# Kernel optimization log

Measured on AMD Instinct MI355X. Metric: run time of the kernel, lower is better.

Reference implementation:

```python
import jax, jax.numpy as jnp
import numpy as np


def gcn_conv(x, W, b, src, dst, n_nodes):
    """PyG-style GCNConv: x' = D^{-1/2}(A+I)D^{-1/2} X W + b, with self-loops added."""
    h = x @ W  # [N, F_out]
    # add self-loops
    loop = jnp.arange(n_nodes, dtype=src.dtype)
    s = jnp.concatenate([src, loop])  # [E+N]
    d = jnp.concatenate([dst, loop])  # [E+N]
    # symmetric normalization: deg counted over incoming edges (incl. self-loops)
    deg = jax.ops.segment_sum(jnp.ones_like(d, dtype=h.dtype), d, num_segments=n_nodes)
    dinv = jnp.where(deg > 0, jax.lax.rsqrt(deg), 0.0)
    coef = dinv[s] * dinv[d]  # [E+N]
    msg = h[s] * coef[:, None]  # gather + scale, [E+N, F_out]
    out = jax.ops.segment_sum(msg, d, num_segments=n_nodes)  # scatter-add
    return out + b


def setup_inputs() -> dict:
    key = jax.random.key(0)
    ks = jax.random.split(key, 6)
    N, E, F_IN, F_HID, F_OUT = 50000, 800000, 128, 128, 64
    x = jax.random.normal(ks[0], (N, F_IN), dtype=jnp.float32)
    edge_index = jax.random.randint(ks[1], (2, E), 0, N, dtype=jnp.int64)
    W0 = jax.random.normal(ks[2], (F_IN, F_HID), dtype=jnp.float32) * (F_IN ** -0.5)
    b0 = jnp.zeros((F_HID,), dtype=jnp.float32)
    W1 = jax.random.normal(ks[3], (F_HID, F_HID), dtype=jnp.float32) * (F_HID ** -0.5)
    b1 = jnp.zeros((F_HID,), dtype=jnp.float32)
    W2 = jax.random.normal(ks[4], (F_HID, F_OUT), dtype=jnp.float32) * (F_HID ** -0.5)
    b2 = jnp.zeros((F_OUT,), dtype=jnp.float32)
    return {"x": x, "edge_index": edge_index, "W0": W0, "b0": b0,
            "W1": W1, "b1": b1, "W2": W2, "b2": b2}


def reference(x, edge_index, W0, b0, W1, b1, W2, b2):
    n_nodes = x.shape[0]
    src, dst = edge_index[0], edge_index[1]
    # hidden GCNConv layers with relu (dropout is identity in eval mode)
    h = jax.nn.relu(gcn_conv(x, W0, b0, src, dst, n_nodes))
    h = jax.nn.relu(gcn_conv(h, W1, b1, src, dst, n_nodes))
    # final conv, no activation
    return gcn_conv(h, W2, b2, src, dst, n_nodes)
```

## Files before the change

kernel.cpp:

```cpp
#include <hip/hip_runtime.h>
#include <hip/hip_fp16.h>
#include <type_traits>

#define F_IN 128
#define NPART 8

typedef _Float16 f16x8 __attribute__((ext_vector_type(8)));
typedef _Float16 f16x4 __attribute__((ext_vector_type(4)));
typedef _Float16 f16x2 __attribute__((ext_vector_type(2)));
typedef float f32x4 __attribute__((ext_vector_type(4)));


__global__ void setup_kernel(const float* __restrict__ W0, const float* __restrict__ W1,
                             const float* __restrict__ W2, __half* __restrict__ Wt0,
                             __half* __restrict__ Wt1, __half* __restrict__ Wt2,
                             int* __restrict__ deg, int N) {
    int idx = blockIdx.x * 256 + threadIdx.x;
    if (idx < 16384) {
        int k = idx >> 7, n = idx & 127;
        Wt0[n * 128 + k] = __float2half_rn(W0[idx]);
    } else if (idx < 32768) {
        int j = idx - 16384;
        int k = j >> 7, n = j & 127;
        Wt1[n * 128 + k] = __float2half_rn(W1[j]);
    } else if (idx < 40960) {
        int j = idx - 32768;
        int k = j >> 6, n = j & 63;
        Wt2[n * 128 + k] = __float2half_rn(W2[j]);
    }
    if (idx < N) deg[idx] = 0;
}


__global__ __launch_bounds__(256) void deg_part_kernel(
    const int* __restrict__ dst, int* __restrict__ deg, int E, int psize)
{
    const int part  = blockIdx.x % NPART;
    const int bslot = blockIdx.x / NPART;
    const int nb    = gridDim.x / NPART;
    const int lo = part * psize;
    const int hi = lo + psize;
    for (int e = bslot * 256 + threadIdx.x; e < E; e += nb * 256) {
        int d = dst[e];
        if (d >= lo && d < hi) atomicAdd(&deg[d], 1);
    }
}


__global__ void scan_blocks(const int* __restrict__ deg, int* __restrict__ rp,
                            int* __restrict__ bsum, int N) {
    __shared__ int tmp[256];
    int t = threadIdx.x, i = blockIdx.x * 256 + t;
    int v = (i < N) ? deg[i] : 0;
    tmp[t] = v;
    __syncthreads();
    for (int off = 1; off < 256; off <<= 1) {
        int a = (t >= off) ? tmp[t - off] : 0;
        __syncthreads();
        tmp[t] += a;
        __syncthreads();
    }
    if (i < N) rp[i] = tmp[t] - v;
    if (t == 255) bsum[blockIdx.x] = tmp[255];
}

__global__ void scan_bsum(int* __restrict__ bsum, int nb) {
    __shared__ int tmp[256];
    int t = threadIdx.x;
    int v = (t < nb) ? bsum[t] : 0;
    tmp[t] = v;
    __syncthreads();
    for (int off = 1; off < 256; off <<= 1) {
        int a = (t >= off) ? tmp[t - off] : 0;
        __syncthreads();
        tmp[t] += a;
        __syncthreads();
    }
    if (t < nb) bsum[t] = tmp[t] - v;
}

__global__ void add_offsets_kernel(int* __restrict__ rp, const int* __restrict__ bsum,
                                   int* __restrict__ cursor, const int* __restrict__ deg,
                                   float* __restrict__ dinv, int N) {
    int i = blockIdx.x * 256 + threadIdx.x;
    if (i < N) {
        int r = rp[i] + bsum[blockIdx.x];
        rp[i] = r;
        cursor[i] = r;
        dinv[i] = rsqrtf((float)(deg[i] + 1));
    }
}

__global__ __launch_bounds__(256) void build_csr_kernel(
    const int* __restrict__ src, const int* __restrict__ dst,
    int* __restrict__ cursor, unsigned short* __restrict__ csr_src,
    int E, int psize)
{
    const int part  = blockIdx.x % NPART;
    const int bslot = blockIdx.x / NPART;
    const int nb    = gridDim.x / NPART;
    const int lo = part * psize;
    const int hi = lo + psize;
    for (int e = bslot * 256 + threadIdx.x; e < E; e += nb * 256) {
        int d = dst[e];
        if (d >= lo && d < hi) {
            int pos = atomicAdd(&cursor[d], 1);
            csr_src[pos] = (unsigned short)src[e];
        }
    }
}


template<int BN, typename XT>
__global__ __launch_bounds__(256) void gemm_mfma_kernel(
    const XT* __restrict__ X, const __half* __restrict__ Wt,
    const float* __restrict__ dinv, __half* __restrict__ g, int N)
{
    constexpr int K  = 128;
    constexpr int KP = K + 8;
    constexpr int NT = BN / 16;
    __shared__ __half Ws[BN * KP];

    const int tid = threadIdx.x;
    for (int c = tid; c < BN * (K / 8); c += 256) {
        int n  = c >> 4;
        int k8 = c & 15;
        *(f16x8*)&Ws[n * KP + k8 * 8] =
            *(const f16x8*)((const _Float16*)Wt + n * K + k8 * 8);
    }
    __syncthreads();

    const int lane = tid & 63;
    const int w    = tid >> 6;
    const int lrow = lane & 15;
    const int kg   = lane >> 4;
    const int row0 = blockIdx.x * 64 + w * 16;
    const int gr   = row0 + lrow;

    f32x4 acc[NT];
    #pragma unroll
    for (int t = 0; t < NT; ++t) acc[t] = (f32x4){0.f, 0.f, 0.f, 0.f};

    #pragma unroll
    for (int ks = 0; ks < 4; ++ks) {
        const int k0 = ks * 32 + kg * 8;
        f16x8 a = {};
        if constexpr (sizeof(XT) == 4) {
            if (gr < N) {
                const float* p = (const float*)X + (size_t)gr * K + k0;
                float4 x0 = *(const float4*)p;
                float4 x1 = *(const float4*)(p + 4);
                a[0] = (_Float16)x0.x; a[1] = (_Float16)x0.y;
                a[2] = (_Float16)x0.z; a[3] = (_Float16)x0.w;
                a[4] = (_Float16)x1.x; a[5] = (_Float16)x1.y;
                a[6] = (_Float16)x1.z; a[7] = (_Float16)x1.w;
            }
        } else {
            if (gr < N)
                a = *(const f16x8*)((const _Float16*)X + (size_t)gr * K + k0);
        }
        #pragma unroll
        for (int t = 0; t < NT; ++t) {
            f16x8 b = *(const f16x8*)&Ws[(t * 16 + lrow) * KP + k0];
            acc[t] = __builtin_amdgcn_mfma_f32_16x16x32_f16(a, b, acc[t], 0, 0, 0);
        }
    }

    #pragma unroll
    for (int r = 0; r < 4; ++r) {
        int m = row0 + kg * 4 + r;
        if (m < N) {
            float dn = dinv[m];
            #pragma unroll
            for (int t = 0; t < NT; ++t)
                g[(size_t)m * BN + t * 16 + lrow] = __float2half_rn(dn * acc[t][r]);
        }
    }
}


template<int FO, bool RELU, typename OT>
__global__ __launch_bounds__(256) void aggregate_kernel(
    const __half* __restrict__ g, const int* __restrict__ rp, const int* __restrict__ deg,
    const unsigned short* __restrict__ csr, const float* __restrict__ dinv,
    const float* __restrict__ bias, OT* __restrict__ out, int N)
{
    constexpr int PER = FO / 32;
    using VT = typename std::conditional<PER == 4, f16x4, f16x2>::type;

    int gid  = blockIdx.x * 256 + threadIdx.x;
    int node = gid >> 5;
    int lane = gid & 31;
    if (node >= N) return;

    int start = rp[node];
    int dg    = deg[node];

    const _Float16* gb = (const _Float16*)g + (size_t)lane * PER;

    float a[PER];
    {
        VT v = *(const VT*)(gb + (size_t)node * FO);
        #pragma unroll
        for (int p = 0; p < PER; ++p) a[p] = (float)v[p];
    }

    int j = 0;
    for (; j + 3 < dg; j += 4) {
        int s0 = csr[start + j];
        int s1 = csr[start + j + 1];
        int s2 = csr[start + j + 2];
        int s3 = csr[start + j + 3];
        VT v0 = *(const VT*)(gb + (size_t)s0 * FO);
        VT v1 = *(const VT*)(gb + (size_t)s1 * FO);
        VT v2 = *(const VT*)(gb + (size_t)s2 * FO);
        VT v3 = *(const VT*)(gb + (size_t)s3 * FO);
        #pragma unroll
        for (int p = 0; p < PER; ++p)
            a[p] += ((float)v0[p] + (float)v1[p]) + ((float)v2[p] + (float)v3[p]);
    }
    for (; j < dg; ++j) {
        int s0 = csr[start + j];
        VT v0 = *(const VT*)(gb + (size_t)s0 * FO);
        #pragma unroll
        for (int p = 0; p < PER; ++p) a[p] += (float)v0[p];
    }

    float dn = dinv[node];
    float o[PER];
    #pragma unroll
    for (int p = 0; p < PER; ++p) {
        o[p] = fmaf(dn, a[p], bias[lane * PER + p]);
        if (RELU) o[p] = fmaxf(o[p], 0.f);
    }

    if constexpr (sizeof(OT) == 2) {
        VT h;
        #pragma unroll
        for (int p = 0; p < PER; ++p) h[p] = (_Float16)o[p];
        *(VT*)((_Float16*)out + (size_t)node * FO + lane * PER) = h;
    } else {
        float* op = (float*)out + (size_t)node * FO + lane * PER;
        if constexpr (PER == 4) {
            *(float4*)op = make_float4(o[0], o[1], o[2], o[3]);
        } else {
            *(float2*)op = make_float2(o[0], o[1]);
        }
    }
}


extern "C" void kernel_launch(void* const* d_in, const int* in_sizes, int n_in,
                              void* d_out, int out_size, void* d_ws, size_t ws_size,
                              hipStream_t stream) {
    const float* x  = (const float*)d_in[0];
    const int*   ei = (const int*)d_in[1];
    const float* W0 = (const float*)d_in[2];
    const float* b0 = (const float*)d_in[3];
    const float* W1 = (const float*)d_in[4];
    const float* b1 = (const float*)d_in[5];
    const float* W2 = (const float*)d_in[6];
    const float* b2 = (const float*)d_in[7];
    float* out = (float*)d_out;

    const int N = in_sizes[0] / F_IN;
    const int E = in_sizes[1] / 2;
    const int* src = ei;
    const int* dst = ei + E;

    char* ws = (char*)d_ws;
    size_t off = 0;
    __half* bufA  = (__half*)(ws + off); off += (size_t)N * 128 * 2;
    __half* bufB  = (__half*)(ws + off); off += (size_t)N * 128 * 2;
    float* dinv   = (float*)(ws + off); off += (size_t)N * 4;
    int*   deg    = (int*)  (ws + off); off += (size_t)N * 4;
    int*   rowptr = (int*)  (ws + off); off += (size_t)N * 4;
    int*   cursor = (int*)  (ws + off); off += (size_t)N * 4;
    int*   bsum   = (int*)  (ws + off); off += 256 * 4;
    unsigned short* csr = (unsigned short*)(ws + off); off += (size_t)E * 2;
    off = (off + 255) & ~(size_t)255;
    __half* wt0 = (__half*)(ws + off); off += 128 * 128 * 2;
    __half* wt1 = (__half*)(ws + off); off += 128 * 128 * 2;
    __half* wt2 = (__half*)(ws + off); off += 64 * 128 * 2;

    const int nb_nodes = (N + 255) / 256;
    const int nb_setup = (((N > 40960 ? N : 40960) + 255) / 256);
    const int nb_aggr  = (N * 32 + 255) / 256;
    const int nb_gemm  = (N + 63) / 64;
    const int psize    = (N + NPART - 1) / NPART;

    setup_kernel<<<nb_setup, 256, 0, stream>>>(W0, W1, W2, wt0, wt1, wt2, deg, N);
    deg_part_kernel<<<NPART * 128, 256, 0, stream>>>(dst, deg, E, psize);
    scan_blocks<<<nb_nodes, 256, 0, stream>>>(deg, rowptr, bsum, N);
    scan_bsum<<<1, 256, 0, stream>>>(bsum, nb_nodes);
    add_offsets_kernel<<<nb_nodes, 256, 0, stream>>>(rowptr, bsum, cursor, deg, dinv, N);
    build_csr_kernel<<<NPART * 128, 256, 0, stream>>>(src, dst, cursor, csr, E, psize);

    gemm_mfma_kernel<128, float><<<nb_gemm, 256, 0, stream>>>(x, wt0, dinv, bufA, N);
    aggregate_kernel<128, true, __half><<<nb_aggr, 256, 0, stream>>>(bufA, rowptr, deg, csr, dinv, b0, bufB, N);

    gemm_mfma_kernel<128, __half><<<nb_gemm, 256, 0, stream>>>(bufB, wt1, dinv, bufA, N);
    aggregate_kernel<128, true, __half><<<nb_aggr, 256, 0, stream>>>(bufA, rowptr, deg, csr, dinv, b1, bufB, N);

    gemm_mfma_kernel<64, __half><<<nb_gemm, 256, 0, stream>>>(bufB, wt2, dinv, bufA, N);
    aggregate_kernel<64, false, float><<<nb_aggr, 256, 0, stream>>>(bufA, rowptr, deg, csr, dinv, b2, out, N);
}
```

Measured before the change: 211.1 us.

## Fuse aggregation with next-layer GEMM via shared memory and merge scan kernels

Each hidden-layer aggregation now writes its ReLU'd fp16 rows into an LDS tile, and the next layer's MFMA GEMM runs in the same block. This removes the intermediate global write and re-read of the activations and two kernel launches. The scan_bsum kernel is dropped: each add_offsets block reduces the preceding block sums itself. In exchange, aggregation gets 64 nodes per block with 8 nodes per pass instead of a flat grid. The extra LDS may also cut occupancy.

```diff
diff --git a/kernel.cpp b/kernel.cpp
--- a/kernel.cpp
+++ b/kernel.cpp
@@ -64,27 +64,21 @@
     if (t == 255) bsum[blockIdx.x] = tmp[255];
 }
 
-__global__ void scan_bsum(int* __restrict__ bsum, int nb) {
+__global__ void add_offsets_kernel(int* __restrict__ rp, const int* __restrict__ bsum,
+                                   int* __restrict__ cursor, const int* __restrict__ deg,
+                                   float* __restrict__ dinv, int N, int nb) {
     __shared__ int tmp[256];
     int t = threadIdx.x;
-    int v = (t < nb) ? bsum[t] : 0;
-    tmp[t] = v;
+    tmp[t] = (t < nb && t < (int)blockIdx.x) ? bsum[t] : 0;
     __syncthreads();
-    for (int off = 1; off < 256; off <<= 1) {
-        int a = (t >= off) ? tmp[t - off] : 0;
+    for (int s = 128; s > 0; s >>= 1) {
+        if (t < s) tmp[t] += tmp[t + s];
         __syncthreads();
-        tmp[t] += a;
-        __syncthreads();
-    }
-    if (t < nb) bsum[t] = tmp[t] - v;
-}
-
-__global__ void add_offsets_kernel(int* __restrict__ rp, const int* __restrict__ bsum,
-                                   int* __restrict__ cursor, const int* __restrict__ deg,
-                                   float* __restrict__ dinv, int N) {
-    int i = blockIdx.x * 256 + threadIdx.x;
+    }
+    int base = tmp[0];
+    int i = blockIdx.x * 256 + t;
     if (i < N) {
-        int r = rp[i] + bsum[blockIdx.x];
+        int r = rp[i] + base;
         rp[i] = r;
         cursor[i] = r;
         dinv[i] = rsqrtf((float)(deg[i] + 1));
@@ -111,13 +105,13 @@
 }
 
 
-template<int BN, typename XT>
-__global__ __launch_bounds__(256) void gemm_mfma_kernel(
-    const XT* __restrict__ X, const __half* __restrict__ Wt,
+__global__ __launch_bounds__(256) void gemm_mfma_l0_kernel(
+    const float* __restrict__ X, const __half* __restrict__ Wt,
     const float* __restrict__ dinv, __half* __restrict__ g, int N)
 {
     constexpr int K  = 128;
     constexpr int KP = K + 8;
+    constexpr int BN = 128;
     constexpr int NT = BN / 16;
     __shared__ __half Ws[BN * KP];
 
@@ -145,19 +139,14 @@
     for (int ks = 0; ks < 4; ++ks) {
         const int k0 = ks * 32 + kg * 8;
         f16x8 a = {};
-        if constexpr (sizeof(XT) == 4) {
-            if (gr < N) {
-                const float* p = (const float*)X + (size_t)gr * K + k0;
-                float4 x0 = *(const float4*)p;
-                float4 x1 = *(const float4*)(p + 4);
-                a[0] = (_Float16)x0.x; a[1] = (_Float16)x0.y;
-                a[2] = (_Float16)x0.z; a[3] = (_Float16)x0.w;
-                a[4] = (_Float16)x1.x; a[5] = (_Float16)x1.y;
-                a[6] = (_Float16)x1.z; a[7] = (_Float16)x1.w;
-            }
-        } else {
-            if (gr < N)
-                a = *(const f16x8*)((const _Float16*)X + (size_t)gr * K + k0);
+        if (gr < N) {
+            const float* p = X + (size_t)gr * K + k0;
+            float4 x0 = *(const float4*)p;
+            float4 x1 = *(const float4*)(p + 4);
+            a[0] = (_Float16)x0.x; a[1] = (_Float16)x0.y;
+            a[2] = (_Float16)x0.z; a[3] = (_Float16)x0.w;
+            a[4] = (_Float16)x1.x; a[5] = (_Float16)x1.y;
+            a[6] = (_Float16)x1.z; a[7] = (_Float16)x1.w;
         }
         #pragma unroll
         for (int t = 0; t < NT; ++t) {
@@ -179,15 +168,116 @@
 }
 
 
-template<int FO, bool RELU, typename OT>
-__global__ __launch_bounds__(256) void aggregate_kernel(
+template<int BN>
+__global__ __launch_bounds__(256) void fused_agg_gemm_kernel(
+    const __half* __restrict__ gin, const int* __restrict__ rp,
+    const int* __restrict__ deg, const unsigned short* __restrict__ csr,
+    const float* __restrict__ dinv, const float* __restrict__ bias,
+    const __half* __restrict__ Wt, __half* __restrict__ gout, int N)
+{
+    constexpr int K  = 128;
+    constexpr int KP = K + 8;
+    constexpr int XP = K + 8;
+    constexpr int NT = BN / 16;
+    __shared__ __half Ws[BN * KP];
+    __shared__ __half Xl[64 * XP];
+
+    const int tid = threadIdx.x;
+    for (int c = tid; c < BN * (K / 8); c += 256) {
+        int n  = c >> 4;
+        int k8 = c & 15;
+        *(f16x8*)&Ws[n * KP + k8 * 8] =
+            *(const f16x8*)((const _Float16*)Wt + n * K + k8 * 8);
+    }
+
+    const int row0 = blockIdx.x * 64;
+    const int grp  = tid >> 5;
+    const int ln   = tid & 31;
+    const _Float16* gb = (const _Float16*)gin + (size_t)ln * 4;
+
+    #pragma unroll 2
+    for (int pass = 0; pass < 8; ++pass) {
+        int nloc = pass * 8 + grp;
+        int node = row0 + nloc;
+        float o[4] = {0.f, 0.f, 0.f, 0.f};
+        if (node < N) {
+            int start = rp[node];
+            int dg    = deg[node];
+            f16x4 sv = *(const f16x4*)(gb + (size_t)node * 128);
+            float a[4];
+            #pragma unroll
+            for (int p = 0; p < 4; ++p) a[p] = (float)sv[p];
+            int j = 0;
+            for (; j + 3 < dg; j += 4) {
+                int s0 = csr[start + j];
+                int s1 = csr[start + j + 1];
+                int s2 = csr[start + j + 2];
+                int s3 = csr[start + j + 3];
+                f16x4 v0 = *(const f16x4*)(gb + (size_t)s0 * 128);
+                f16x4 v1 = *(const f16x4*)(gb + (size_t)s1 * 128);
+                f16x4 v2 = *(const f16x4*)(gb + (size_t)s2 * 128);
+                f16x4 v3 = *(const f16x4*)(gb + (size_t)s3 * 128);
+                #pragma unroll
+                for (int p = 0; p < 4; ++p)
+                    a[p] += ((float)v0[p] + (float)v1[p]) + ((float)v2[p] + (float)v3[p]);
+            }
+            for (; j < dg; ++j) {
+                int s0 = csr[start + j];
+                f16x4 v0 = *(const f16x4*)(gb + (size_t)s0 * 128);
+                #pragma unroll
+                for (int p = 0; p < 4; ++p) a[p] += (float)v0[p];
+            }
+            float dn = dinv[node];
+            #pragma unroll
+            for (int p = 0; p < 4; ++p)
+                o[p] = fmaxf(fmaf(dn, a[p], bias[ln * 4 + p]), 0.f);
+        }
+        f16x4 h;
+        #pragma unroll
+        for (int p = 0; p < 4; ++p) h[p] = (_Float16)o[p];
+        *(f16x4*)&Xl[nloc * XP + ln * 4] = h;
+    }
+    __syncthreads();
+
+    const int lane = tid & 63;
+    const int w    = tid >> 6;
+    const int lrow = lane & 15;
+    const int kg   = lane >> 4;
+
+    f32x4 acc[NT];
+    #pragma unroll
+    for (int t = 0; t < NT; ++t) acc[t] = (f32x4){0.f, 0.f, 0.f, 0.f};
+
+    #pragma unroll
+    for (int ks = 0; ks < 4; ++ks) {
+        const int k0 = ks * 32 + kg * 8;
+        f16x8 a = *(const f16x8*)&Xl[(w * 16 + lrow) * XP + k0];
+        #pragma unroll
+        for (int t = 0; t < NT; ++t) {
+            f16x8 b = *(const f16x8*)&Ws[(t * 16 + lrow) * KP + k0];
+            acc[t] = __builtin_amdgcn_mfma_f32_16x16x32_f16(a, b, acc[t], 0, 0, 0);
+        }
+    }
+
+    #pragma unroll
+    for (int r = 0; r < 4; ++r) {
+        int m = row0 + w * 16 + kg * 4 + r;
+        if (m < N) {
+            float dn = dinv[m];
+            #pragma unroll
+            for (int t = 0; t < NT; ++t)
+                gout[(size_t)m * BN + t * 16 + lrow] = __float2half_rn(dn * acc[t][r]);
+        }
+    }
+}
+
+
+__global__ __launch_bounds__(256) void aggregate_final_kernel(
     const __half* __restrict__ g, const int* __restrict__ rp, const int* __restrict__ deg,
     const unsigned short* __restrict__ csr, const float* __restrict__ dinv,
-    const float* __restrict__ bias, OT* __restrict__ out, int N)
-{
-    constexpr int PER = FO / 32;
-    using VT = typename std::conditional<PER == 4, f16x4, f16x2>::type;
-
+    const float* __restrict__ bias, float* __restrict__ out, int N)
+{
+    constexpr int FO = 64, PER = 2;
     int gid  = blockIdx.x * 256 + threadIdx.x;
     int node = gid >> 5;
     int lane = gid & 31;
@@ -200,7 +290,7 @@
 
     float a[PER];
     {
-        VT v = *(const VT*)(gb + (size_t)node * FO);
+        f16x2 v = *(const f16x2*)(gb + (size_t)node * FO);
         #pragma unroll
         for (int p = 0; p < PER; ++p) a[p] = (float)v[p];
     }
@@ -211,42 +301,26 @@
         int s1 = csr[start + j + 1];
         int s2 = csr[start + j + 2];
         int s3 = csr[start + j + 3];
-        VT v0 = *(const VT*)(gb + (size_t)s0 * FO);
-        VT v1 = *(const VT*)(gb + (size_t)s1 * FO);
-        VT v2 = *(const VT*)(gb + (size_t)s2 * FO);
-        VT v3 = *(const VT*)(gb + (size_t)s3 * FO);
+        f16x2 v0 = *(const f16x2*)(gb + (size_t)s0 * FO);
+        f16x2 v1 = *(const f16x2*)(gb + (size_t)s1 * FO);
+        f16x2 v2 = *(const f16x2*)(gb + (size_t)s2 * FO);
+        f16x2 v3 = *(const f16x2*)(gb + (size_t)s3 * FO);
         #pragma unroll
         for (int p = 0; p < PER; ++p)
             a[p] += ((float)v0[p] + (float)v1[p]) + ((float)v2[p] + (float)v3[p]);
     }
     for (; j < dg; ++j) {
         int s0 = csr[start + j];
-        VT v0 = *(const VT*)(gb + (size_t)s0 * FO);
+        f16x2 v0 = *(const f16x2*)(gb + (size_t)s0 * FO);
         #pragma unroll
         for (int p = 0; p < PER; ++p) a[p] += (float)v0[p];
     }
 
     float dn = dinv[node];
-    float o[PER];
-    #pragma unroll
-    for (int p = 0; p < PER; ++p) {
-        o[p] = fmaf(dn, a[p], bias[lane * PER + p]);
-        if (RELU) o[p] = fmaxf(o[p], 0.f);
-    }
-
-    if constexpr (sizeof(OT) == 2) {
-        VT h;
-        #pragma unroll
-        for (int p = 0; p < PER; ++p) h[p] = (_Float16)o[p];
-        *(VT*)((_Float16*)out + (size_t)node * FO + lane * PER) = h;
-    } else {
-        float* op = (float*)out + (size_t)node * FO + lane * PER;
-        if constexpr (PER == 4) {
-            *(float4*)op = make_float4(o[0], o[1], o[2], o[3]);
-        } else {
-            *(float2*)op = make_float2(o[0], o[1]);
-        }
-    }
+    float2 o;
+    o.x = fmaf(dn, a[0], bias[lane * PER]);
+    o.y = fmaf(dn, a[1], bias[lane * PER + 1]);
+    *(float2*)(out + (size_t)node * FO + lane * PER) = o;
 }
 
 
@@ -271,7 +345,7 @@
     char* ws = (char*)d_ws;
     size_t off = 0;
     __half* bufA  = (__half*)(ws + off); off += (size_t)N * 128 * 2;
-    __half* bufB  = (__half*)(ws + off); off += (size_t)N * 128 * 2;
+    __half* bufC  = (__half*)(ws + off); off += (size_t)N * 128 * 2;
     float* dinv   = (float*)(ws + off); off += (size_t)N * 4;
     int*   deg    = (int*)  (ws + off); off += (size_t)N * 4;
     int*   rowptr = (int*)  (ws + off); off += (size_t)N * 4;
@@ -292,16 +366,11 @@
     setup_kernel<<<nb_setup, 256, 0, stream>>>(W0, W1, W2, wt0, wt1, wt2, deg, N);
     deg_part_kernel<<<NPART * 128, 256, 0, stream>>>(dst, deg, E, psize);
     scan_blocks<<<nb_nodes, 256, 0, stream>>>(deg, rowptr, bsum, N);
-    scan_bsum<<<1, 256, 0, stream>>>(bsum, nb_nodes);
-    add_offsets_kernel<<<nb_nodes, 256, 0, stream>>>(rowptr, bsum, cursor, deg, dinv, N);
+    add_offsets_kernel<<<nb_nodes, 256, 0, stream>>>(rowptr, bsum, cursor, deg, dinv, N, nb_nodes);
     build_csr_kernel<<<NPART * 128, 256, 0, stream>>>(src, dst, cursor, csr, E, psize);
 
-    gemm_mfma_kernel<128, float><<<nb_gemm, 256, 0, stream>>>(x, wt0, dinv, bufA, N);
-    aggregate_kernel<128, true, __half><<<nb_aggr, 256, 0, stream>>>(bufA, rowptr, deg, csr, dinv, b0, bufB, N);
-
-    gemm_mfma_kernel<128, __half><<<nb_gemm, 256, 0, stream>>>(bufB, wt1, dinv, bufA, N);
-    aggregate_kernel<128, true, __half><<<nb_aggr, 256, 0, stream>>>(bufA, rowptr, deg, csr, dinv, b1, bufB, N);
-
-    gemm_mfma_kernel<64, __half><<<nb_gemm, 256, 0, stream>>>(bufB, wt2, dinv, bufA, N);
-    aggregate_kernel<64, false, float><<<nb_aggr, 256, 0, stream>>>(bufA, rowptr, deg, csr, dinv, b2, out, N);
-}
+    gemm_mfma_l0_kernel<<<nb_gemm, 256, 0, stream>>>(x, wt0, dinv, bufA, N);
+    fused_agg_gemm_kernel<128><<<nb_gemm, 256, 0, stream>>>(bufA, rowptr, deg, csr, dinv, b0, wt1, bufC, N);
+    fused_agg_gemm_kernel<64><<<nb_gemm, 256, 0, stream>>>(bufC, rowptr, deg, csr, dinv, b1, wt2, bufA, N);
+    aggregate_final_kernel<<<nb_aggr, 256, 0, stream>>>(bufA, rowptr, deg, csr, dinv, b2, out, N);
+}
```

After: 257.1 us. 1.22x slower.
